# Kernel optimization log

Measured on AMD Instinct MI355X. Metric: run time of the kernel, lower is better.

The kernel has to match this reference:

```python
import jax, jax.numpy as jnp
import numpy as np

B, F, D, U = 4096, 32, 64, 256


def setup_inputs() -> dict:
    key = jax.random.key(0)
    k1, k2, k3, k4 = jax.random.split(key, 4)
    embeds = jax.random.normal(k1, (B, F, D), dtype=jnp.float32)
    # glorot-ish scaling for the learned weights
    linear_w = jax.random.normal(k2, (F * D, U), dtype=jnp.float32) * (2.0 / (F * D + U)) ** 0.5
    inner_w = jax.random.normal(k3, (U, F), dtype=jnp.float32) * (2.0 / (U + F)) ** 0.5
    outer_w = jax.random.normal(k4, (U, D, D), dtype=jnp.float32) * (2.0 / (2 * D)) ** 0.5
    return {"embeds": embeds, "linear_w": linear_w, "inner_w": inner_w, "outer_w": outer_w}


def reference(embeds, linear_w, inner_w, outer_w):
    b = embeds.shape[0]
    # linear signal lz: flatten fields and project -> [B, U]
    lz = embeds.reshape(b, -1) @ linear_w
    # inner products: per unit u, delta_u = sum_f w_{u,f} * e_f  -> [B, U, D];
    # lp_inner[b,u] = ||delta_u||^2 (collapses the per-unit TF loop into one einsum)
    delta = jnp.einsum('bfd,uf->bud', embeds, inner_w)
    lp_inner = jnp.sum(jnp.square(delta), axis=2)  # [B, U]
    # outer products: product = fs fs^T with fs = sum_f e_f; lp_outer[b,u] = <product_b, W_u>
    fs = jnp.sum(embeds, axis=1)  # [B, D]
    lp_outer = jnp.einsum('bi,bj,uij->bu', fs, fs, outer_w)  # [B, U]
    return jnp.concatenate([lz, lp_inner, lp_outer], axis=1)  # [B, 3U]
```

## Files before the change

### kernel.cpp

```cpp
#include <hip/hip_runtime.h>
#include <hip/hip_bf16.h>


#define KA 3072
#define KW 7168

typedef __attribute__((ext_vector_type(8))) short short8v;
typedef __attribute__((ext_vector_type(4))) float f32x4;

#define GLOAD(src, dst) __builtin_amdgcn_global_load_lds( \
    (const __attribute__((address_space(1))) void*)(src), \
    (__attribute__((address_space(3))) void*)(dst), 16, 0, 0)

static __device__ __forceinline__ short f2bf(float f) {
    union { float f; unsigned u; } v; v.f = f;
    unsigned r = v.u + 0x7fffu + ((v.u >> 16) & 1u);
    return (short)(r >> 16);
}
static __device__ __forceinline__ float bf2f(short s) {
    union { unsigned u; float f; } v; v.u = ((unsigned)(unsigned short)s) << 16;
    return v.f;
}
static __device__ __forceinline__ int cvtpk(float lo, float hi) {
    int r;
    asm("v_cvt_pk_bf16_f32 %0, %1, %2" : "=v"(r) : "v"(lo), "v"(hi));
    return r;
}

__global__ __launch_bounds__(256) void prep_a(const float* __restrict__ embeds,
                                              short* __restrict__ A,
                                              short* __restrict__ FS) {
    int b = blockIdx.x;
    const float* e = embeds + (size_t)b * 2048;
    short* arow = A + (size_t)b * KA;
    __shared__ float se[2048];
    __shared__ short sebf[2048];
    int t = threadIdx.x;

    float4 v0 = ((const float4*)e)[t * 2];
    float4 v1 = ((const float4*)e)[t * 2 + 1];
    ((float4*)se)[t * 2] = v0;
    ((float4*)se)[t * 2 + 1] = v1;
    short8v sb;
    sb[0] = f2bf(v0.x); sb[1] = f2bf(v0.y); sb[2] = f2bf(v0.z); sb[3] = f2bf(v0.w);
    sb[4] = f2bf(v1.x); sb[5] = f2bf(v1.y); sb[6] = f2bf(v1.z); sb[7] = f2bf(v1.w);
    ((short8v*)sebf)[t] = sb;
    *(short8v*)&arow[t * 8] = sb;

    __syncthreads();
    if (t < 64) {
        float s = 0.f;
        #pragma unroll
        for (int f = 0; f < 32; ++f) s += se[f * 64 + t];
        FS[(size_t)b * 64 + t] = f2bf(s);
    }

    int wid = t >> 6, lane = t & 63;
    int tm = wid >> 1, tn = wid & 1;
    int lr = lane & 15, lk = (lane >> 4) * 8;
    f32x4 g = {0.f, 0.f, 0.f, 0.f};
    #pragma unroll
    for (int ks = 0; ks < 2; ++ks) {
        short8v a  = *(const short8v*)&sebf[(tm * 16 + lr) * 64 + ks * 32 + lk];
        short8v bb = *(const short8v*)&sebf[(tn * 16 + lr) * 64 + ks * 32 + lk];
        g = __builtin_amdgcn_mfma_f32_16x16x32_bf16(a, bb, g, 0, 0, 0);
    }
    #pragma unroll
    for (int r = 0; r < 4; ++r) {
        int grow = tm * 16 + (lane >> 4) * 4 + r;
        int gcol = tn * 16 + lr;
        arow[2048 + grow * 32 + gcol] = f2bf(g[r]);
    }
}

__global__ __launch_bounds__(256) void prep_w(const float* __restrict__ lw,
                                              const float* __restrict__ iw,
                                              const float* __restrict__ ow,
                                              short* __restrict__ Wt) {
    int u = blockIdx.x;
    int t = threadIdx.x;
    short* w = Wt + (size_t)u * KW;

    for (int k = t; k < 2048; k += 256) w[k] = f2bf(lw[(size_t)k * 256 + u]);

    __shared__ float wi[32];
    if (t < 32) wi[t] = iw[u * 32 + t];
    __syncthreads();
    for (int idx = t; idx < 1024; idx += 256)
        w[2048 + idx] = f2bf(wi[idx >> 5] * wi[idx & 31]);

    const float* owu = ow + (size_t)u * 4096;
    for (int i = t; i < 512; i += 256) {
        float4 a = ((const float4*)owu)[i * 2];
        float4 b = ((const float4*)owu)[i * 2 + 1];
        short8v s;
        s[0] = f2bf(a.x); s[1] = f2bf(a.y); s[2] = f2bf(a.z); s[3] = f2bf(a.w);
        s[4] = f2bf(b.x); s[5] = f2bf(b.y); s[6] = f2bf(b.z); s[7] = f2bf(b.w);
        *(short8v*)&w[3072 + i * 8] = s;
    }
}

__global__ __launch_bounds__(256) void gemm_tile(const short* __restrict__ A,
                                                 const short* __restrict__ Wt,
                                                 const short* __restrict__ FS,
                                                 float* __restrict__ out) {
    __shared__ short As[2][16384];
    __shared__ short Bs[2][4096];

    int id = blockIdx.x;
    int mt = id >> 5, r5 = id & 31, nt = r5 >> 3, c8 = r5 & 7;
    int seg, kc;
    if (c8 < 2)      { seg = 0; kc = c8; }
    else if (c8 < 4) { seg = 1; kc = c8 - 2; }
    else             { seg = 2; kc = c8 - 4; }
    const int nk = (seg == 1) ? 8 : 16;
    int brow = mt * 256, bcol = nt * 64;
    int akoff = (seg == 0) ? kc * 1024 : 2048 + kc * 512;
    int boff  = (seg == 0) ? kc * 1024 : (seg == 1) ? 2048 + kc * 512 : 3072 + kc * 1024;

    int t = threadIdx.x, w = t >> 6, lane = t & 63;
    int lr = lane & 15, hi = lane >> 4;
    int srow = t >> 3;
    int soct = (t & 7) ^ (srow & 7);

    const short* Asrc = A  + (size_t)(brow + srow) * KA + akoff + soct * 8;
    const short* Bsrc = Wt + (size_t)(bcol + srow) * KW + boff  + soct * 8;
    const short* Fsrc = FS + (size_t)(brow + srow) * 64 + soct * 8;

    auto stageA = [&](int p, int kt) {
        #pragma unroll
        for (int i = 0; i < 8; ++i)
            GLOAD(Asrc + (size_t)i * 32 * KA + kt * 64, &As[p][i * 2048 + t * 8]);
    };
    auto stageB = [&](int p, int kt) {
        #pragma unroll
        for (int i = 0; i < 2; ++i)
            GLOAD(Bsrc + (size_t)i * 32 * KW + kt * 64, &Bs[p][i * 2048 + t * 8]);
    };

    f32x4 acc[4][4];
    #pragma unroll
    for (int m = 0; m < 4; ++m)
        #pragma unroll
        for (int n = 0; n < 4; ++n) acc[m][n] = (f32x4){0.f, 0.f, 0.f, 0.f};

    if (seg == 2) {
        #pragma unroll
        for (int i = 0; i < 8; ++i)
            GLOAD(Fsrc + (size_t)i * 32 * 64, &As[0][i * 2048 + t * 8]);
        stageB(0, 0);
    } else {
        stageA(0, 0); stageB(0, 0);
    }
    __syncthreads();

    if (seg != 2) {
        for (int kt = 0; kt < nk; ++kt) {
            int cur = kt & 1;
            if (kt + 1 < nk) { stageA(cur ^ 1, kt + 1); stageB(cur ^ 1, kt + 1); }
            #pragma unroll
            for (int ks = 0; ks < 2; ++ks) {
                int oct = ((ks * 4 + hi) ^ (lr & 7)) * 8;
                short8v a[4], b[4];
                #pragma unroll
                for (int m = 0; m < 4; ++m)
                    a[m] = *(const short8v*)&As[cur][(w * 64 + m * 16 + lr) * 64 + oct];
                #pragma unroll
                for (int n = 0; n < 4; ++n)
                    b[n] = *(const short8v*)&Bs[cur][(n * 16 + lr) * 64 + oct];
                #pragma unroll
                for (int m = 0; m < 4; ++m)
                    #pragma unroll
                    for (int n = 0; n < 4; ++n)
                        acc[m][n] = __builtin_amdgcn_mfma_f32_16x16x32_bf16(a[m], b[n], acc[m][n], 0, 0, 0);
            }
            __syncthreads();
        }
    } else {
        float fj[4][2][8];
        #pragma unroll
        for (int m = 0; m < 4; ++m)
            #pragma unroll
            for (int ks = 0; ks < 2; ++ks) {
                int oct = ((ks * 4 + hi) ^ (lr & 7)) * 8;
                short8v v = *(const short8v*)&As[0][(w * 64 + m * 16 + lr) * 64 + oct];
                #pragma unroll
                for (int e = 0; e < 8; ++e) fj[m][ks][e] = bf2f(v[e]);
            }
        for (int kt = 0; kt < nk; ++kt) {
            int cur = kt & 1;
            if (kt + 1 < nk) stageB(cur ^ 1, kt + 1);
            int iidx = kc * 16 + kt;
            int ioff = ((iidx >> 3) ^ (lr & 7)) * 8 + (iidx & 7);
            float s[4];
            #pragma unroll
            for (int m = 0; m < 4; ++m)
                s[m] = bf2f(As[0][(w * 64 + m * 16 + lr) * 64 + ioff]);
            #pragma unroll
            for (int ks = 0; ks < 2; ++ks) {
                int oct = ((ks * 4 + hi) ^ (lr & 7)) * 8;
                short8v b[4];
                #pragma unroll
                for (int n = 0; n < 4; ++n)
                    b[n] = *(const short8v*)&Bs[cur][(n * 16 + lr) * 64 + oct];
                #pragma unroll
                for (int m = 0; m < 4; ++m) {
                    union { int i32[4]; short8v v; } fa;
                    #pragma unroll
                    for (int q = 0; q < 4; ++q)
                        fa.i32[q] = cvtpk(s[m] * fj[m][ks][2 * q], s[m] * fj[m][ks][2 * q + 1]);
                    #pragma unroll
                    for (int n = 0; n < 4; ++n)
                        acc[m][n] = __builtin_amdgcn_mfma_f32_16x16x32_bf16(fa.v, b[n], acc[m][n], 0, 0, 0);
                }
            }
            __syncthreads();
        }
    }

    int segbase = seg * 256;
    #pragma unroll
    for (int m = 0; m < 4; ++m) {
        int row0 = brow + w * 64 + m * 16 + hi * 4;
        #pragma unroll
        for (int n = 0; n < 4; ++n) {
            int col = segbase + bcol + n * 16 + lr;
            #pragma unroll
            for (int r = 0; r < 4; ++r)
                unsafeAtomicAdd(&out[(size_t)(row0 + r) * 768 + col], acc[m][n][r]);
        }
    }
}

extern "C" void kernel_launch(void* const* d_in, const int* in_sizes, int n_in,
                              void* d_out, int out_size, void* d_ws, size_t ws_size,
                              hipStream_t stream) {
    const float* embeds = (const float*)d_in[0];
    const float* lw = (const float*)d_in[1];
    const float* iw = (const float*)d_in[2];
    const float* ow = (const float*)d_in[3];
    float* out = (float*)d_out;

    short* A  = (short*)d_ws;
    short* Wt = A + (size_t)4096 * KA;
    short* FS = Wt + (size_t)256 * KW;

    hipMemsetAsync(out, 0, (size_t)out_size * sizeof(float), stream);
    prep_a<<<dim3(4096), dim3(256), 0, stream>>>(embeds, A, FS);
    prep_w<<<dim3(256), dim3(256), 0, stream>>>(lw, iw, ow, Wt);
    gemm_tile<<<dim3(512), dim3(256), 0, stream>>>(A, Wt, FS, out);
}
```

Measured before the change: 65.21 us.

## Merge prep kernels, drop split-K atomics and memset with 128-row tiles

New measurement: 65.83 us. No clear change (+0.9%).

```diff
diff --git a/kernel.cpp b/kernel.cpp
--- a/kernel.cpp
+++ b/kernel.cpp
@@ -27,76 +27,76 @@
     return r;
 }
 
-__global__ __launch_bounds__(256) void prep_a(const float* __restrict__ embeds,
-                                              short* __restrict__ A,
-                                              short* __restrict__ FS) {
-    int b = blockIdx.x;
-    const float* e = embeds + (size_t)b * 2048;
-    short* arow = A + (size_t)b * KA;
+__global__ __launch_bounds__(256) void prep(const float* __restrict__ embeds,
+                                            const float* __restrict__ lw,
+                                            const float* __restrict__ iw,
+                                            const float* __restrict__ ow,
+                                            short* __restrict__ A,
+                                            short* __restrict__ FS,
+                                            short* __restrict__ Wt) {
     __shared__ float se[2048];
     __shared__ short sebf[2048];
     int t = threadIdx.x;
 
-    float4 v0 = ((const float4*)e)[t * 2];
-    float4 v1 = ((const float4*)e)[t * 2 + 1];
-    ((float4*)se)[t * 2] = v0;
-    ((float4*)se)[t * 2 + 1] = v1;
-    short8v sb;
-    sb[0] = f2bf(v0.x); sb[1] = f2bf(v0.y); sb[2] = f2bf(v0.z); sb[3] = f2bf(v0.w);
-    sb[4] = f2bf(v1.x); sb[5] = f2bf(v1.y); sb[6] = f2bf(v1.z); sb[7] = f2bf(v1.w);
-    ((short8v*)sebf)[t] = sb;
-    *(short8v*)&arow[t * 8] = sb;
-
-    __syncthreads();
-    if (t < 64) {
-        float s = 0.f;
-        #pragma unroll
-        for (int f = 0; f < 32; ++f) s += se[f * 64 + t];
-        FS[(size_t)b * 64 + t] = f2bf(s);
-    }
-
-    int wid = t >> 6, lane = t & 63;
-    int tm = wid >> 1, tn = wid & 1;
-    int lr = lane & 15, lk = (lane >> 4) * 8;
-    f32x4 g = {0.f, 0.f, 0.f, 0.f};
-    #pragma unroll
-    for (int ks = 0; ks < 2; ++ks) {
-        short8v a  = *(const short8v*)&sebf[(tm * 16 + lr) * 64 + ks * 32 + lk];
-        short8v bb = *(const short8v*)&sebf[(tn * 16 + lr) * 64 + ks * 32 + lk];
-        g = __builtin_amdgcn_mfma_f32_16x16x32_bf16(a, bb, g, 0, 0, 0);
-    }
-    #pragma unroll
-    for (int r = 0; r < 4; ++r) {
-        int grow = tm * 16 + (lane >> 4) * 4 + r;
-        int gcol = tn * 16 + lr;
-        arow[2048 + grow * 32 + gcol] = f2bf(g[r]);
-    }
-}
-
-__global__ __launch_bounds__(256) void prep_w(const float* __restrict__ lw,
-                                              const float* __restrict__ iw,
-                                              const float* __restrict__ ow,
-                                              short* __restrict__ Wt) {
-    int u = blockIdx.x;
-    int t = threadIdx.x;
-    short* w = Wt + (size_t)u * KW;
-
-    for (int k = t; k < 2048; k += 256) w[k] = f2bf(lw[(size_t)k * 256 + u]);
-
-    __shared__ float wi[32];
-    if (t < 32) wi[t] = iw[u * 32 + t];
-    __syncthreads();
-    for (int idx = t; idx < 1024; idx += 256)
-        w[2048 + idx] = f2bf(wi[idx >> 5] * wi[idx & 31]);
-
-    const float* owu = ow + (size_t)u * 4096;
-    for (int i = t; i < 512; i += 256) {
-        float4 a = ((const float4*)owu)[i * 2];
-        float4 b = ((const float4*)owu)[i * 2 + 1];
-        short8v s;
-        s[0] = f2bf(a.x); s[1] = f2bf(a.y); s[2] = f2bf(a.z); s[3] = f2bf(a.w);
-        s[4] = f2bf(b.x); s[5] = f2bf(b.y); s[6] = f2bf(b.z); s[7] = f2bf(b.w);
-        *(short8v*)&w[3072 + i * 8] = s;
+    if (blockIdx.x < 4096) {
+        int b = blockIdx.x;
+        const float* e = embeds + (size_t)b * 2048;
+        short* arow = A + (size_t)b * KA;
+
+        float4 v0 = ((const float4*)e)[t * 2];
+        float4 v1 = ((const float4*)e)[t * 2 + 1];
+        ((float4*)se)[t * 2] = v0;
+        ((float4*)se)[t * 2 + 1] = v1;
+        short8v sb;
+        sb[0] = f2bf(v0.x); sb[1] = f2bf(v0.y); sb[2] = f2bf(v0.z); sb[3] = f2bf(v0.w);
+        sb[4] = f2bf(v1.x); sb[5] = f2bf(v1.y); sb[6] = f2bf(v1.z); sb[7] = f2bf(v1.w);
+        ((short8v*)sebf)[t] = sb;
+        *(short8v*)&arow[t * 8] = sb;
+
+        __syncthreads();
+        if (t < 64) {
+            float s = 0.f;
+            #pragma unroll
+            for (int f = 0; f < 32; ++f) s += se[f * 64 + t];
+            FS[(size_t)b * 64 + t] = f2bf(s);
+        }
+
+        int wid = t >> 6, lane = t & 63;
+        int tm = wid >> 1, tn = wid & 1;
+        int lr = lane & 15, lk = (lane >> 4) * 8;
+        f32x4 g = {0.f, 0.f, 0.f, 0.f};
+        #pragma unroll
+        for (int ks = 0; ks < 2; ++ks) {
+            short8v a  = *(const short8v*)&sebf[(tm * 16 + lr) * 64 + ks * 32 + lk];
+            short8v bb = *(const short8v*)&sebf[(tn * 16 + lr) * 64 + ks * 32 + lk];
+            g = __builtin_amdgcn_mfma_f32_16x16x32_bf16(a, bb, g, 0, 0, 0);
+        }
+        #pragma unroll
+        for (int r = 0; r < 4; ++r) {
+            int grow = tm * 16 + (lane >> 4) * 4 + r;
+            int gcol = tn * 16 + lr;
+            arow[2048 + grow * 32 + gcol] = f2bf(g[r]);
+        }
+    } else {
+        int u = blockIdx.x - 4096;
+        short* w = Wt + (size_t)u * KW;
+
+        for (int k = t; k < 2048; k += 256) w[k] = f2bf(lw[(size_t)k * 256 + u]);
+
+        if (t < 32) se[t] = iw[u * 32 + t];
+        __syncthreads();
+        for (int idx = t; idx < 1024; idx += 256)
+            w[2048 + idx] = f2bf(se[idx >> 5] * se[idx & 31]);
+
+        const float* owu = ow + (size_t)u * 4096;
+        for (int i = t; i < 512; i += 256) {
+            float4 a = ((const float4*)owu)[i * 2];
+            float4 b = ((const float4*)owu)[i * 2 + 1];
+            short8v s;
+            s[0] = f2bf(a.x); s[1] = f2bf(a.y); s[2] = f2bf(a.z); s[3] = f2bf(a.w);
+            s[4] = f2bf(b.x); s[5] = f2bf(b.y); s[6] = f2bf(b.z); s[7] = f2bf(b.w);
+            *(short8v*)&w[3072 + i * 8] = s;
+        }
     }
 }
 
@@ -104,19 +104,19 @@
                                                  const short* __restrict__ Wt,
                                                  const short* __restrict__ FS,
                                                  float* __restrict__ out) {
-    __shared__ short As[2][16384];
+    __shared__ short As[2][8192];
     __shared__ short Bs[2][4096];
 
     int id = blockIdx.x;
-    int mt = id >> 5, r5 = id & 31, nt = r5 >> 3, c8 = r5 & 7;
-    int seg, kc;
-    if (c8 < 2)      { seg = 0; kc = c8; }
-    else if (c8 < 4) { seg = 1; kc = c8 - 2; }
-    else             { seg = 2; kc = c8 - 4; }
-    const int nk = (seg == 1) ? 8 : 16;
-    int brow = mt * 256, bcol = nt * 64;
-    int akoff = (seg == 0) ? kc * 1024 : 2048 + kc * 512;
-    int boff  = (seg == 0) ? kc * 1024 : (seg == 1) ? 2048 + kc * 512 : 3072 + kc * 1024;
+    int seg, loc;
+    if (id < 128)      { seg = 0; loc = id; }
+    else if (id < 256) { seg = 2; loc = id - 128; }
+    else               { seg = 1; loc = id - 256; }
+    int mt = loc >> 2, nt = loc & 3;
+    const int nk = (seg == 0) ? 32 : (seg == 1) ? 16 : 64;
+    int brow = mt * 128, bcol = nt * 64;
+    int akoff = (seg == 1) ? 2048 : 0;
+    int boff  = (seg == 0) ? 0 : (seg == 1) ? 2048 : 3072;
 
     int t = threadIdx.x, w = t >> 6, lane = t & 63;
     int lr = lane & 15, hi = lane >> 4;
@@ -129,7 +129,7 @@
 
     auto stageA = [&](int p, int kt) {
         #pragma unroll
-        for (int i = 0; i < 8; ++i)
+        for (int i = 0; i < 4; ++i)
             GLOAD(Asrc + (size_t)i * 32 * KA + kt * 64, &As[p][i * 2048 + t * 8]);
     };
     auto stageB = [&](int p, int kt) {
@@ -138,15 +138,15 @@
             GLOAD(Bsrc + (size_t)i * 32 * KW + kt * 64, &Bs[p][i * 2048 + t * 8]);
     };
 
-    f32x4 acc[4][4];
+    f32x4 acc[2][4];
     #pragma unroll
-    for (int m = 0; m < 4; ++m)
+    for (int m = 0; m < 2; ++m)
         #pragma unroll
         for (int n = 0; n < 4; ++n) acc[m][n] = (f32x4){0.f, 0.f, 0.f, 0.f};
 
     if (seg == 2) {
         #pragma unroll
-        for (int i = 0; i < 8; ++i)
+        for (int i = 0; i < 4; ++i)
             GLOAD(Fsrc + (size_t)i * 32 * 64, &As[0][i * 2048 + t * 8]);
         stageB(0, 0);
     } else {
@@ -161,15 +161,15 @@
             #pragma unroll
             for (int ks = 0; ks < 2; ++ks) {
                 int oct = ((ks * 4 + hi) ^ (lr & 7)) * 8;
-                short8v a[4], b[4];
-                #pragma unroll
-                for (int m = 0; m < 4; ++m)
-                    a[m] = *(const short8v*)&As[cur][(w * 64 + m * 16 + lr) * 64 + oct];
+                short8v a[2], b[4];
+                #pragma unroll
+                for (int m = 0; m < 2; ++m)
+                    a[m] = *(const short8v*)&As[cur][(w * 32 + m * 16 + lr) * 64 + oct];
                 #pragma unroll
                 for (int n = 0; n < 4; ++n)
                     b[n] = *(const short8v*)&Bs[cur][(n * 16 + lr) * 64 + oct];
                 #pragma unroll
-                for (int m = 0; m < 4; ++m)
+                for (int m = 0; m < 2; ++m)
                     #pragma unroll
                     for (int n = 0; n < 4; ++n)
                         acc[m][n] = __builtin_amdgcn_mfma_f32_16x16x32_bf16(a[m], b[n], acc[m][n], 0, 0, 0);
@@ -177,25 +177,24 @@
             __syncthreads();
         }
     } else {
-        float fj[4][2][8];
-        #pragma unroll
-        for (int m = 0; m < 4; ++m)
+        float fj[2][2][8];
+        #pragma unroll
+        for (int m = 0; m < 2; ++m)
             #pragma unroll
             for (int ks = 0; ks < 2; ++ks) {
                 int oct = ((ks * 4 + hi) ^ (lr & 7)) * 8;
-                short8v v = *(const short8v*)&As[0][(w * 64 + m * 16 + lr) * 64 + oct];
+                short8v v = *(const short8v*)&As[0][(w * 32 + m * 16 + lr) * 64 + oct];
                 #pragma unroll
                 for (int e = 0; e < 8; ++e) fj[m][ks][e] = bf2f(v[e]);
             }
-        for (int kt = 0; kt < nk; ++kt) {
+        for (int kt = 0; kt < 64; ++kt) {
             int cur = kt & 1;
-            if (kt + 1 < nk) stageB(cur ^ 1, kt + 1);
-            int iidx = kc * 16 + kt;
-            int ioff = ((iidx >> 3) ^ (lr & 7)) * 8 + (iidx & 7);
-            float s[4];
-            #pragma unroll
-            for (int m = 0; m < 4; ++m)
-                s[m] = bf2f(As[0][(w * 64 + m * 16 + lr) * 64 + ioff]);
+            if (kt + 1 < 64) stageB(cur ^ 1, kt + 1);
+            int ioff = ((kt >> 3) ^ (lr & 7)) * 8 + (kt & 7);
+            float s[2];
+            #pragma unroll
+            for (int m = 0; m < 2; ++m)
+                s[m] = bf2f(As[0][(w * 32 + m * 16 + lr) * 64 + ioff]);
             #pragma unroll
             for (int ks = 0; ks < 2; ++ks) {
                 int oct = ((ks * 4 + hi) ^ (lr & 7)) * 8;
@@ -204,7 +203,7 @@
                 for (int n = 0; n < 4; ++n)
                     b[n] = *(const short8v*)&Bs[cur][(n * 16 + lr) * 64 + oct];
                 #pragma unroll
-                for (int m = 0; m < 4; ++m) {
+                for (int m = 0; m < 2; ++m) {
                     union { int i32[4]; short8v v; } fa;
                     #pragma unroll
                     for (int q = 0; q < 4; ++q)
@@ -220,14 +219,14 @@
 
     int segbase = seg * 256;
     #pragma unroll
-    for (int m = 0; m < 4; ++m) {
-        int row0 = brow + w * 64 + m * 16 + hi * 4;
+    for (int m = 0; m < 2; ++m) {
+        int row0 = brow + w * 32 + m * 16 + hi * 4;
         #pragma unroll
         for (int n = 0; n < 4; ++n) {
             int col = segbase + bcol + n * 16 + lr;
             #pragma unroll
             for (int r = 0; r < 4; ++r)
-                unsafeAtomicAdd(&out[(size_t)(row0 + r) * 768 + col], acc[m][n][r]);
+                out[(size_t)(row0 + r) * 768 + col] = acc[m][n][r];
         }
     }
 }
@@ -245,8 +244,6 @@
     short* Wt = A + (size_t)4096 * KA;
     short* FS = Wt + (size_t)256 * KW;
 
-    hipMemsetAsync(out, 0, (size_t)out_size * sizeof(float), stream);
-    prep_a<<<dim3(4096), dim3(256), 0, stream>>>(embeds, A, FS);
-    prep_w<<<dim3(256), dim3(256), 0, stream>>>(lw, iw, ow, Wt);
-    gemm_tile<<<dim3(512), dim3(256), 0, stream>>>(A, Wt, FS, out);
-}
+    prep<<<dim3(4352), dim3(256), 0, stream>>>(embeds, lw, iw, ow, A, FS, Wt);
+    gemm_tile<<<dim3(384), dim3(256), 0, stream>>>(A, Wt, FS, out);
+}
```
